# Kernel tuning notes

Hardware: AMD Instinct MI355X
Metric: run time of the kernel (lower is better)

Reference implementation:

```python
import jax, jax.numpy as jnp
import numpy as np

F_SIZE = 32
H_DIM = 540
W_DIM = 960
T_DIM = 300
HID1 = 64
FEAT = 64
HID2X2 = 256
UV_L = 10
T_L = 6
BLOCK2_IN = FEAT + (UV_L * 2 * 2 + 2) + (T_L * 2 + 1)  # 119
N_PTS = 1048576


def plane_sample(plane, uv):
    """Bilinear grid_sample, align_corners=False, padding_mode='border'.
    plane: (f, H, W); uv: (N, 2) in [0,1]; uv[:,0] samples W, uv[:,1] samples H
    (matches torch grid last-dim (x, y) convention). Returns (N, f)."""
    f, H, W = plane.shape
    g = uv * 2.0 - 1.0
    u, v = g[:, 0], g[:, 1]
    # unnormalize (align_corners=False) then border-clamp the coordinate
    ix = jnp.clip(((u + 1.0) * W - 1.0) * 0.5, 0.0, W - 1.0)
    iy = jnp.clip(((v + 1.0) * H - 1.0) * 0.5, 0.0, H - 1.0)
    x0f = jnp.floor(ix)
    y0f = jnp.floor(iy)
    wx = ix - x0f
    wy = iy - y0f
    x0 = x0f.astype(jnp.int32)
    y0 = y0f.astype(jnp.int32)
    x1 = jnp.minimum(x0 + 1, W - 1)
    y1 = jnp.minimum(y0 + 1, H - 1)
    v00 = plane[:, y0, x0]  # (f, N)
    v01 = plane[:, y0, x1]
    v10 = plane[:, y1, x0]
    v11 = plane[:, y1, x1]
    out = (v00 * (1 - wx) * (1 - wy) + v01 * wx * (1 - wy)
           + v10 * (1 - wx) * wy + v11 * wx * wy)
    return out.T  # (N, f)


def pos_enc(x, L):
    outs = [x]
    for j in range(L):
        s = (2.0 ** j) * x
        outs.append(jnp.sin(s))
        outs.append(jnp.cos(s))
    return jnp.concatenate(outs, axis=-1)


def _linear_params(key, fan_in, fan_out):
    kw, kb = jax.random.split(key)
    scale = 1.0 / np.sqrt(fan_in)
    W = jax.random.uniform(kw, (fan_in, fan_out), minval=-scale, maxval=scale, dtype=jnp.float32)
    b = jax.random.uniform(kb, (fan_out,), minval=-scale, maxval=scale, dtype=jnp.float32)
    return W, b


def setup_inputs() -> dict:
    key = jax.random.key(0)
    ks = jax.random.split(key, 10)
    xyt = jax.random.uniform(ks[0], (N_PTS, 3), dtype=jnp.float32)
    xyt = xyt.at[:, 2].multiply(300.0)  # t in [0, frames_num)
    yx_plane = jax.random.uniform(ks[1], (F_SIZE, H_DIM, W_DIM), dtype=jnp.float32)
    xt_plane = jax.random.uniform(ks[2], (F_SIZE, W_DIM, T_DIM), dtype=jnp.float32)
    yt_plane = jax.random.uniform(ks[3], (F_SIZE, H_DIM, T_DIM), dtype=jnp.float32)
    fw1, fb1 = _linear_params(ks[4], F_SIZE, HID1)
    fw2, fb2 = _linear_params(ks[5], HID1, FEAT)
    w1, b1 = _linear_params(ks[6], BLOCK2_IN, HID2X2)
    w2, b2 = _linear_params(ks[7], HID2X2, HID2X2)
    w3, b3 = _linear_params(ks[8], HID2X2, HID2X2)
    w4, b4 = _linear_params(ks[9], HID2X2, 3)
    return {"xyt": xyt, "yx_plane": yx_plane, "xt_plane": xt_plane,
            "yt_plane": yt_plane, "fw1": fw1, "fb1": fb1, "fw2": fw2,
            "fb2": fb2, "w1": w1, "b1": b1, "w2": w2, "b2": b2,
            "w3": w3, "b3": b3, "w4": w4, "b4": b4, "frames_num": 300}


def reference(xyt, yx_plane, xt_plane, yt_plane, fw1, fb1, fw2, fb2,
              w1, b1, w2, b2, w3, b3, w4, b4, frames_num):
    x = xyt[:, 0:1]
    y = xyt[:, 1:2]
    t = xyt[:, 2:3] / frames_num
    yx_f = plane_sample(yx_plane, jnp.concatenate([y, x], axis=-1))
    xt_f = plane_sample(xt_plane, jnp.concatenate([x, t], axis=-1))
    yt_f = plane_sample(yt_plane, jnp.concatenate([y, t], axis=-1))
    feat = yx_f * xt_f * yt_f  # (N, f_size)
    h = jax.nn.relu(feat @ fw1 + fb1)
    h = jax.nn.relu(h @ fw2 + fb2)
    yx_pe = pos_enc(jnp.concatenate([y, x], axis=-1), UV_L)
    t_pe = pos_enc(t, T_L)
    full = jnp.concatenate([h, yx_pe, t_pe], axis=-1)  # (N, 119)
    z = jax.nn.relu(full @ w1 + b1)
    z = jax.nn.relu(z @ w2 + b2)
    z = jax.nn.relu(z @ w3 + b3)
    colors = jax.nn.sigmoid(z @ w4 + b4)  # (N, 3)
    return colors
```

## Files before the change

kernel.cpp:

```cpp
#include <hip/hip_runtime.h>

typedef __bf16 bf16_t;
typedef __bf16 bf16x8 __attribute__((ext_vector_type(8)));
typedef _Float16 f16x4 __attribute__((ext_vector_type(4)));
typedef unsigned short u16x8 __attribute__((ext_vector_type(8)));
typedef unsigned short u16x4 __attribute__((ext_vector_type(4)));
typedef float f32x4 __attribute__((ext_vector_type(4)));

#define MT 64
#define NTHR 512
#define NBLK (1048576 / MT)

__device__ __forceinline__ int swz(int row, int colbyte) {
  return row * 512 + (colbyte ^ ((row & 31) << 4));
}
__device__ __forceinline__ void st_act(unsigned short* buf, int row, int col, float v) {
  buf[swz(row, col * 2) >> 1] = __builtin_bit_cast(unsigned short, (bf16_t)v);
}
__device__ __forceinline__ void st_act4(unsigned short* buf, int row, int col, float v0, float v1,
                                        float v2, float v3) {
  u16x4 pk;
  pk[0] = __builtin_bit_cast(unsigned short, (bf16_t)v0);
  pk[1] = __builtin_bit_cast(unsigned short, (bf16_t)v1);
  pk[2] = __builtin_bit_cast(unsigned short, (bf16_t)v2);
  pk[3] = __builtin_bit_cast(unsigned short, (bf16_t)v3);
  *reinterpret_cast<uint2*>(reinterpret_cast<char*>(buf) + swz(row, col * 2)) =
      __builtin_bit_cast(uint2, pk);
}
__device__ __forceinline__ bf16x8 ld_frag(const unsigned short* buf, int row, int kbyte) {
  const uint4 u =
      *reinterpret_cast<const uint4*>(reinterpret_cast<const char*>(buf) + swz(row, kbyte));
  return __builtin_bit_cast(bf16x8, u);
}

__global__ void KPlanes_tr3(const float* __restrict__ yx, const float* __restrict__ xt,
                            const float* __restrict__ yt, uint4* __restrict__ d0,
                            uint4* __restrict__ d1, uint4* __restrict__ d2) {
  const int HW0 = 518400, HW1 = 288000, HW2 = 162000;
  const int NB0 = 2025, NB1 = 1125;
  const int b = blockIdx.x;
  const float* src;
  uint4* dst;
  int HW, s;
  if (b < NB0) {
    src = yx; dst = d0; HW = HW0; s = b * 256 + threadIdx.x;
  } else if (b < NB0 + NB1) {
    src = xt; dst = d1; HW = HW1; s = (b - NB0) * 256 + threadIdx.x;
  } else {
    src = yt; dst = d2; HW = HW2; s = (b - NB0 - NB1) * 256 + threadIdx.x;
  }
  if (s >= HW) return;
#pragma unroll
  for (int g = 0; g < 4; ++g) {
    u16x8 v;
#pragma unroll
    for (int j = 0; j < 8; ++j) {
      const float w = src[(size_t)(g * 8 + j) * HW + s];
      v[j] = __builtin_bit_cast(unsigned short, (_Float16)w);
    }
    dst[(size_t)s * 4 + g] = __builtin_bit_cast(uint4, v);
  }
}

__global__ void KPlanes_packall(const float* __restrict__ fw1, const float* __restrict__ fw2,
                                const float* __restrict__ w1, const float* __restrict__ w2,
                                const float* __restrict__ w3, const float* __restrict__ w4,
                                uint4* __restrict__ dst) {
  const int F = blockIdx.x * 4 + (threadIdx.x >> 6);
  const int lane = threadIdx.x & 63;
  if (F >= 340) return;
  const float* W;
  int N, K, KS, fbase;
  if (F < 4)        { W = fw1; N = 64;  K = 32;  KS = 1; fbase = 0; }
  else if (F < 12)  { W = fw2; N = 64;  K = 64;  KS = 2; fbase = 4; }
  else if (F < 76)  { W = w1;  N = 256; K = 119; KS = 4; fbase = 12; }
  else if (F < 204) { W = w2;  N = 256; K = 256; KS = 8; fbase = 76; }
  else if (F < 332) { W = w3;  N = 256; K = 256; KS = 8; fbase = 204; }
  else              { W = w4;  N = 3;   K = 256; KS = 8; fbase = 332; }
  const int f = F - fbase;
  const int g = f / KS, ks = f - g * KS;
  const int col = g * 16 + (lane & 15);
  u16x8 v;
#pragma unroll
  for (int j = 0; j < 8; ++j) {
    const int k = ks * 32 + (lane >> 4) * 8 + j;
    const float w = (k < K && col < N) ? W[(size_t)k * N + col] : 0.0f;
    v[j] = __builtin_bit_cast(unsigned short, (bf16_t)w);
  }
  dst[(size_t)F * 64 + lane] = __builtin_bit_cast(uint4, v);
}

struct Smp4 {
  uint2 c00, c01, c10, c11;
  float w00, w01, w10, w11;
};
__device__ __forceinline__ Smp4 sample_ld4(const uint2* __restrict__ plt, int Hd, int Wd, float u,
                                           float v, int q) {
  Smp4 s;
  float ix = fminf(fmaxf(u * (float)Wd - 0.5f, 0.f), (float)Wd - 1.f);
  float iy = fminf(fmaxf(v * (float)Hd - 0.5f, 0.f), (float)Hd - 1.f);
  float x0f = floorf(ix), y0f = floorf(iy);
  float wx = ix - x0f, wy = iy - y0f;
  int x0 = (int)x0f, y0 = (int)y0f;
  int x1 = min(x0 + 1, Wd - 1), y1 = min(y0 + 1, Hd - 1);
  s.w00 = (1.f - wx) * (1.f - wy);
  s.w01 = wx * (1.f - wy);
  s.w10 = (1.f - wx) * wy;
  s.w11 = wx * wy;
  const size_t r0 = (size_t)y0 * Wd, r1 = (size_t)y1 * Wd;
  s.c00 = plt[(r0 + x0) * 8 + q];
  s.c01 = plt[(r0 + x1) * 8 + q];
  s.c10 = plt[(r1 + x0) * 8 + q];
  s.c11 = plt[(r1 + x1) * 8 + q];
  return s;
}
__device__ __forceinline__ void smp_combine4(const Smp4& s, float* o) {
  const f16x4 a = __builtin_bit_cast(f16x4, s.c00);
  const f16x4 b = __builtin_bit_cast(f16x4, s.c01);
  const f16x4 c = __builtin_bit_cast(f16x4, s.c10);
  const f16x4 d = __builtin_bit_cast(f16x4, s.c11);
#pragma unroll
  for (int i = 0; i < 4; ++i)
    o[i] = (float)a[i] * s.w00 + (float)b[i] * s.w01 + (float)c[i] * s.w10 + (float)d[i] * s.w11;
}

template <int KS, int NT, int MTPW, bool RELU>
__device__ __forceinline__ void layer_pp(const unsigned short* in, unsigned short* outb,
                                         const uint4* __restrict__ Wf,
                                         const float* __restrict__ bg, int gbase, int moff,
                                         int lane) {
  const int l15 = lane & 15, lhi = lane >> 4;
  f32x4 acc[MTPW][NT];
#pragma unroll
  for (int m = 0; m < MTPW; ++m)
#pragma unroll
    for (int t = 0; t < NT; ++t) acc[m][t] = f32x4{0.f, 0.f, 0.f, 0.f};
#pragma unroll
  for (int ks = 0; ks < KS; ++ks) {
    bf16x8 wa[NT];
#pragma unroll
    for (int t = 0; t < NT; ++t)
      wa[t] = __builtin_bit_cast(bf16x8, Wf[(size_t)((gbase + t) * KS + ks) * 64 + lane]);
#pragma unroll
    for (int m = 0; m < MTPW; ++m) {
      const bf16x8 b = ld_frag(in, (moff + m) * 16 + l15, ks * 64 + lhi * 16);
#pragma unroll
      for (int t = 0; t < NT; ++t)
        acc[m][t] = __builtin_amdgcn_mfma_f32_16x16x32_bf16(wa[t], b, acc[m][t], 0, 0, 0);
    }
  }
#pragma unroll
  for (int t = 0; t < NT; ++t) {
    const int ncol = (gbase + t) * 16 + lhi * 4;
    const float4 b4 = *reinterpret_cast<const float4*>(&bg[ncol]);
#pragma unroll
    for (int m = 0; m < MTPW; ++m) {
      const int row = (moff + m) * 16 + l15;
      float v0 = acc[m][t][0] + b4.x, v1 = acc[m][t][1] + b4.y;
      float v2 = acc[m][t][2] + b4.z, v3 = acc[m][t][3] + b4.w;
      if (RELU) {
        v0 = fmaxf(v0, 0.f); v1 = fmaxf(v1, 0.f);
        v2 = fmaxf(v2, 0.f); v3 = fmaxf(v3, 0.f);
      }
      st_act4(outb, row, ncol, v0, v1, v2, v3);
    }
  }
}

__global__ __launch_bounds__(NTHR, 4) void KPlanes_fused6(
    const float* __restrict__ xyt, const uint2* __restrict__ yx_h, const uint2* __restrict__ xt_h,
    const uint2* __restrict__ yt_h, const uint4* __restrict__ wf1, const float* __restrict__ fb1,
    const uint4* __restrict__ wf2, const float* __restrict__ fb2, const uint4* __restrict__ wf3,
    const float* __restrict__ b1, const uint4* __restrict__ wf4, const float* __restrict__ b2,
    const uint4* __restrict__ wf5, const float* __restrict__ b3, const uint4* __restrict__ wf6,
    const float* __restrict__ b4, const int* __restrict__ fnum_p, float* __restrict__ out) {
  __shared__ unsigned short actA[MT * 256];
  __shared__ unsigned short actB[MT * 256];
  const int tid = threadIdx.x;
  const int lane = tid & 63;
  const int wid = tid >> 6;
  const float rfn = 1.0f / (float)(*fnum_p);

  {
    const int p = tid >> 3;
    const int q = tid & 7;
    const int pg = blockIdx.x * MT + p;
    const float x = xyt[pg * 3 + 0];
    const float y = xyt[pg * 3 + 1];
    const float t = xyt[pg * 3 + 2] * rfn;
    Smp4 sYX = sample_ld4(yx_h, 540, 960, y, x, q);
    Smp4 sXT = sample_ld4(xt_h, 960, 300, x, t, q);
    Smp4 sYT = sample_ld4(yt_h, 540, 300, y, t, q);
    if (q == 4) {
      st_act(actA, p, 64, y);
      float sj, cj;
      sincosf(y, &sj, &cj);
#pragma unroll
      for (int j = 0; j < 10; ++j) {
        st_act(actA, p, 66 + j * 4, sj);
        st_act(actA, p, 68 + j * 4, cj);
        const float ns = 2.f * sj * cj;
        cj = fmaf(-2.f * sj, sj, 1.f);
        sj = ns;
      }
    } else if (q == 5) {
      st_act(actA, p, 65, x);
      float sj, cj;
      sincosf(x, &sj, &cj);
#pragma unroll
      for (int j = 0; j < 10; ++j) {
        st_act(actA, p, 67 + j * 4, sj);
        st_act(actA, p, 69 + j * 4, cj);
        const float ns = 2.f * sj * cj;
        cj = fmaf(-2.f * sj, sj, 1.f);
        sj = ns;
      }
    } else if (q == 6) {
      st_act(actA, p, 106, t);
      float sj, cj;
      sincosf(t, &sj, &cj);
#pragma unroll
      for (int j = 0; j < 6; ++j) {
        st_act(actA, p, 107 + 2 * j, sj);
        st_act(actA, p, 108 + 2 * j, cj);
        const float ns = 2.f * sj * cj;
        cj = fmaf(-2.f * sj, sj, 1.f);
        sj = ns;
      }
    } else if (q == 7) {
      st_act(actA, p, 119, 0.f);
      st_act4(actA, p, 120, 0.f, 0.f, 0.f, 0.f);
      st_act4(actA, p, 124, 0.f, 0.f, 0.f, 0.f);
    }
    float a4[4], b4_[4], c4[4];
    smp_combine4(sYX, a4);
    smp_combine4(sXT, b4_);
    smp_combine4(sYT, c4);
    st_act4(actA, p, q * 4, a4[0] * b4_[0] * c4[0], a4[1] * b4_[1] * c4[1],
            a4[2] * b4_[2] * c4[2], a4[3] * b4_[3] * c4[3]);
  }
  __syncthreads();
  layer_pp<1, 1, 2, true>(actA, actB, wf1, fb1, wid & 3, (wid >> 2) * 2, lane);
  __syncthreads();
  layer_pp<2, 1, 2, true>(actB, actA, wf2, fb2, wid & 3, (wid >> 2) * 2, lane);
  __syncthreads();
  layer_pp<4, 2, 4, true>(actA, actB, wf3, b1, wid * 2, 0, lane);
  __syncthreads();
  layer_pp<8, 2, 4, true>(actB, actA, wf4, b2, wid * 2, 0, lane);
  __syncthreads();
  layer_pp<8, 2, 4, true>(actA, actB, wf5, b3, wid * 2, 0, lane);
  __syncthreads();
  if (wid < 4) {
    const int l15 = lane & 15, lhi = lane >> 4;
    f32x4 acc = {0.f, 0.f, 0.f, 0.f};
#pragma unroll
    for (int ks = 0; ks < 8; ++ks) {
      const bf16x8 wa = __builtin_bit_cast(bf16x8, wf6[ks * 64 + lane]);
      acc = __builtin_amdgcn_mfma_f32_16x16x32_bf16(
          wa, ld_frag(actB, wid * 16 + l15, ks * 64 + lhi * 16), acc, 0, 0, 0);
    }
    if (lhi == 0) {
      const size_t pg = (size_t)blockIdx.x * MT + wid * 16 + l15;
#pragma unroll
      for (int i = 0; i < 3; ++i) {
        const float v = acc[i] + b4[i];
        out[pg * 3 + i] = 1.f / (1.f + expf(-v));
      }
    }
  }
}

__device__ __forceinline__ void sample8_f(const float* __restrict__ pl, int Hd, int Wd, float u,
                                          float v, int cgrp, float* o) {
  float ix = fminf(fmaxf(u * (float)Wd - 0.5f, 0.f), (float)Wd - 1.f);
  float iy = fminf(fmaxf(v * (float)Hd - 0.5f, 0.f), (float)Hd - 1.f);
  float x0f = floorf(ix), y0f = floorf(iy);
  float wx = ix - x0f, wy = iy - y0f;
  int x0 = (int)x0f, y0 = (int)y0f;
  int x1 = min(x0 + 1, Wd - 1), y1 = min(y0 + 1, Hd - 1);
  float w00 = (1.f - wx) * (1.f - wy), w01 = wx * (1.f - wy);
  float w10 = (1.f - wx) * wy, w11 = wx * wy;
  const size_t HW = (size_t)Hd * Wd;
#pragma unroll
  for (int i = 0; i < 8; ++i) {
    const float* bc = pl + (size_t)(cgrp + i) * HW;
    float a = bc[(size_t)y0 * Wd + x0], b = bc[(size_t)y0 * Wd + x1];
    float c = bc[(size_t)y1 * Wd + x0], d = bc[(size_t)y1 * Wd + x1];
    o[i] = a * w00 + b * w01 + c * w10 + d * w11;
  }
}

template <int KSTEPS, int NCPW, bool RELU>
__device__ __forceinline__ void mfma_layer_fb(const unsigned short* inb, unsigned short* outb,
                                              const float* __restrict__ Wg,
                                              const float* __restrict__ bg, int N, int Kmax,
                                              int wid, int lane) {
  const int l15 = lane & 15;
  const int lhi = lane >> 4;
#pragma unroll
  for (int t = 0; t < NCPW; ++t) {
    const int nc = wid * NCPW + t;
    const int col = nc * 16 + l15;
    const float bias = bg[col];
    bf16x8 bfrag[KSTEPS];
#pragma unroll
    for (int ks = 0; ks < KSTEPS; ++ks) {
#pragma unroll
      for (int j = 0; j < 8; ++j) {
        const int k = ks * 32 + lhi * 8 + j;
        float wv = (k < Kmax) ? Wg[(size_t)k * N + col] : 0.0f;
        bfrag[ks][j] = (bf16_t)wv;
      }
    }
#pragma unroll
    for (int m = 0; m < 4; ++m) {
      f32x4 acc = {0.f, 0.f, 0.f, 0.f};
#pragma unroll
      for (int ks = 0; ks < KSTEPS; ++ks) {
        bf16x8 a = ld_frag(inb, m * 16 + l15, ks * 64 + lhi * 16);
        acc = __builtin_amdgcn_mfma_f32_16x16x32_bf16(a, bfrag[ks], acc, 0, 0, 0);
      }
      const int r0 = m * 16 + lhi * 4;
#pragma unroll
      for (int i = 0; i < 4; ++i) {
        float v = acc[i] + bias;
        if (RELU) v = fmaxf(v, 0.f);
        st_act(outb, r0 + i, col, v);
      }
    }
  }
}

__global__ __launch_bounds__(256) void KPlanes_fused_fb(
    const float* __restrict__ xyt, const float* __restrict__ yx, const float* __restrict__ xt,
    const float* __restrict__ yt, const float* __restrict__ fw1, const float* __restrict__ fb1,
    const float* __restrict__ fw2, const float* __restrict__ fb2, const float* __restrict__ w1,
    const float* __restrict__ b1, const float* __restrict__ w2, const float* __restrict__ b2,
    const float* __restrict__ w3, const float* __restrict__ b3, const float* __restrict__ w4,
    const float* __restrict__ b4, const int* __restrict__ fnum_p, float* __restrict__ out) {
  __shared__ unsigned short actA[64 * 256];
  __shared__ unsigned short actB[64 * 256];
  const int tid = threadIdx.x;
  const int lane = tid & 63;
  const int wid = tid >> 6;
  const float fnum = (float)(*fnum_p);
  {
    const int p = tid >> 2;
    const int cgrp = (tid & 3) * 8;
    const int pg = blockIdx.x * 64 + p;
    float x = xyt[pg * 3 + 0];
    float y = xyt[pg * 3 + 1];
    float t = xyt[pg * 3 + 2] / fnum;
    float syx[8], sxt[8], syt[8];
    sample8_f(yx, 540, 960, y, x, cgrp, syx);
    sample8_f(xt, 960, 300, x, t, cgrp, sxt);
    sample8_f(yt, 540, 300, y, t, cgrp, syt);
#pragma unroll
    for (int i = 0; i < 8; ++i) st_act(actA, p, cgrp + i, syx[i] * sxt[i] * syt[i]);
  }
  __syncthreads();
  mfma_layer_fb<1, 1, true>(actA, actB, fw1, fb1, 64, 32, wid, lane);
  __syncthreads();
  mfma_layer_fb<2, 1, true>(actB, actA, fw2, fb2, 64, 64, wid, lane);
  if (tid < 64) {
    const int pg = blockIdx.x * 64 + tid;
    float px = xyt[pg * 3 + 0];
    float py = xyt[pg * 3 + 1];
    float pt = xyt[pg * 3 + 2] / fnum;
    st_act(actA, tid, 64, py);
    st_act(actA, tid, 65, px);
    float sc = 1.f;
#pragma unroll
    for (int j = 0; j < 10; ++j) {
      st_act(actA, tid, 66 + j * 4 + 0, sinf(sc * py));
      st_act(actA, tid, 66 + j * 4 + 1, sinf(sc * px));
      st_act(actA, tid, 66 + j * 4 + 2, cosf(sc * py));
      st_act(actA, tid, 66 + j * 4 + 3, cosf(sc * px));
      sc *= 2.f;
    }
    st_act(actA, tid, 106, pt);
    sc = 1.f;
#pragma unroll
    for (int j = 0; j < 6; ++j) {
      st_act(actA, tid, 107 + j * 2, sinf(sc * pt));
      st_act(actA, tid, 108 + j * 2, cosf(sc * pt));
      sc *= 2.f;
    }
#pragma unroll
    for (int c = 119; c < 128; ++c) st_act(actA, tid, c, 0.f);
  }
  __syncthreads();
  mfma_layer_fb<4, 4, true>(actA, actB, w1, b1, 256, 119, wid, lane);
  __syncthreads();
  mfma_layer_fb<8, 4, true>(actB, actA, w2, b2, 256, 256, wid, lane);
  __syncthreads();
  mfma_layer_fb<8, 4, true>(actA, actB, w3, b3, 256, 256, wid, lane);
  __syncthreads();
  {
    const int p = tid >> 2, c = tid & 3;
    if (c < 3) {
      float acc = 0.f;
#pragma unroll
      for (int k0 = 0; k0 < 256; k0 += 8) {
        int b = swz(p, k0 * 2);
        uint4 u = *reinterpret_cast<const uint4*>(reinterpret_cast<const char*>(actB) + b);
        bf16x8 z = __builtin_bit_cast(bf16x8, u);
#pragma unroll
        for (int j = 0; j < 8; ++j) acc += (float)z[j] * w4[(k0 + j) * 3 + c];
      }
      acc += b4[c];
      out[(size_t)(blockIdx.x * 64 + p) * 3 + c] = 1.f / (1.f + expf(-acc));
    }
  }
}

extern "C" void kernel_launch(void* const* d_in, const int* in_sizes, int n_in, void* d_out,
                              int out_size, void* d_ws, size_t ws_size, hipStream_t stream) {
  const float* xyt = (const float*)d_in[0];
  const float* yx = (const float*)d_in[1];
  const float* xt = (const float*)d_in[2];
  const float* yt = (const float*)d_in[3];
  const float* fw1 = (const float*)d_in[4];
  const float* fb1 = (const float*)d_in[5];
  const float* fw2 = (const float*)d_in[6];
  const float* fb2 = (const float*)d_in[7];
  const float* w1 = (const float*)d_in[8];
  const float* b1 = (const float*)d_in[9];
  const float* w2 = (const float*)d_in[10];
  const float* b2 = (const float*)d_in[11];
  const float* w3 = (const float*)d_in[12];
  const float* b3 = (const float*)d_in[13];
  const float* w4 = (const float*)d_in[14];
  const float* b4 = (const float*)d_in[15];
  const int* fnum = (const int*)d_in[16];
  float* out = (float*)d_out;

  const int hw_yx = 540 * 960, hw_xt = 960 * 300, hw_yt = 540 * 300;
  const size_t plane_bytes = ((size_t)hw_yx + hw_xt + hw_yt) * 64;
  const size_t wfrag_bytes = (size_t)340 * 64 * sizeof(uint4);
  const size_t need = plane_bytes + wfrag_bytes;

  char* ws = (char*)d_ws;
  uint2* yx_h = (uint2*)ws;
  uint2* xt_h = (uint2*)(ws + (size_t)hw_yx * 64);
  uint2* yt_h = (uint2*)(ws + (size_t)(hw_yx + hw_xt) * 64);
  uint4* wbase = (uint4*)(ws + plane_bytes);
  uint4* wf1 = wbase + 0 * 64;
  uint4* wf2 = wbase + 4 * 64;
  uint4* wf3 = wbase + 12 * 64;
  uint4* wf4 = wbase + 76 * 64;
  uint4* wf5 = wbase + 204 * 64;
  uint4* wf6 = wbase + 332 * 64;

  if (ws_size >= need) {
    const int nb_tr = 2025 + 1125 + 633;
    KPlanes_tr3<<<nb_tr, 256, 0, stream>>>(yx, xt, yt, (uint4*)yx_h, (uint4*)xt_h, (uint4*)yt_h);
    KPlanes_packall<<<85, 256, 0, stream>>>(fw1, fw2, w1, w2, w3, w4, wbase);
    KPlanes_fused6<<<NBLK, NTHR, 0, stream>>>(xyt, yx_h, xt_h, yt_h, wf1, fb1, wf2, fb2, wf3, b1,
                                              wf4, b2, wf5, b3, wf6, b4, fnum, out);
  } else {
    KPlanes_fused_fb<<<1048576 / 64, 256, 0, stream>>>(xyt, yx, xt, yt, fw1, fb1, fw2, fb2, w1,
                                                       b1, w2, b2, w3, b3, w4, b4, fnum, out);
  }
}
```

Before: 476.9 us.

## Store MLP activations in LDS as pre-packed MFMA fragments instead of swizzled rows

```diff
diff --git a/kernel.cpp b/kernel.cpp
--- a/kernel.cpp
+++ b/kernel.cpp
@@ -11,26 +11,21 @@
 #define NTHR 512
 #define NBLK (1048576 / MT)
 
-__device__ __forceinline__ int swz(int row, int colbyte) {
-  return row * 512 + (colbyte ^ ((row & 31) << 4));
-}
-__device__ __forceinline__ void st_act(unsigned short* buf, int row, int col, float v) {
-  buf[swz(row, col * 2) >> 1] = __builtin_bit_cast(unsigned short, (bf16_t)v);
-}
-__device__ __forceinline__ void st_act4(unsigned short* buf, int row, int col, float v0, float v1,
-                                        float v2, float v3) {
+__device__ __forceinline__ int fragoff(int NK, int pg, int n, int p15) {
+  return ((pg * NK + (n >> 5)) << 10) + (((n >> 3) & 3) << 8) + (p15 << 4) + ((n & 7) << 1);
+}
+__device__ __forceinline__ void st_frag1(char* buf, int NK, int pg, int n, int p15, float v) {
+  *reinterpret_cast<unsigned short*>(buf + fragoff(NK, pg, n, p15)) =
+      __builtin_bit_cast(unsigned short, (bf16_t)v);
+}
+__device__ __forceinline__ void st_frag4(char* buf, int NK, int pg, int n, int p15, float v0,
+                                         float v1, float v2, float v3) {
   u16x4 pk;
   pk[0] = __builtin_bit_cast(unsigned short, (bf16_t)v0);
   pk[1] = __builtin_bit_cast(unsigned short, (bf16_t)v1);
   pk[2] = __builtin_bit_cast(unsigned short, (bf16_t)v2);
   pk[3] = __builtin_bit_cast(unsigned short, (bf16_t)v3);
-  *reinterpret_cast<uint2*>(reinterpret_cast<char*>(buf) + swz(row, col * 2)) =
-      __builtin_bit_cast(uint2, pk);
-}
-__device__ __forceinline__ bf16x8 ld_frag(const unsigned short* buf, int row, int kbyte) {
-  const uint4 u =
-      *reinterpret_cast<const uint4*>(reinterpret_cast<const char*>(buf) + swz(row, kbyte));
-  return __builtin_bit_cast(bf16x8, u);
+  *reinterpret_cast<uint2*>(buf + fragoff(NK, pg, n, p15)) = __builtin_bit_cast(uint2, pk);
 }
 
 __global__ void KPlanes_tr3(const float* __restrict__ yx, const float* __restrict__ xt,
@@ -124,12 +119,12 @@
     o[i] = (float)a[i] * s.w00 + (float)b[i] * s.w01 + (float)c[i] * s.w10 + (float)d[i] * s.w11;
 }
 
-template <int KS, int NT, int MTPW, bool RELU>
-__device__ __forceinline__ void layer_pp(const unsigned short* in, unsigned short* outb,
-                                         const uint4* __restrict__ Wf,
+template <int KS, int NKOUT, int NT, int MTPW, bool RELU>
+__device__ __forceinline__ void layer_fp(const char* in, char* outb, const uint4* __restrict__ Wf,
                                          const float* __restrict__ bg, int gbase, int moff,
                                          int lane) {
   const int l15 = lane & 15, lhi = lane >> 4;
+  const char* rb = in + lane * 16 + moff * (KS << 10);
   f32x4 acc[MTPW][NT];
 #pragma unroll
   for (int m = 0; m < MTPW; ++m)
@@ -143,7 +138,8 @@
       wa[t] = __builtin_bit_cast(bf16x8, Wf[(size_t)((gbase + t) * KS + ks) * 64 + lane]);
 #pragma unroll
     for (int m = 0; m < MTPW; ++m) {
-      const bf16x8 b = ld_frag(in, (moff + m) * 16 + l15, ks * 64 + lhi * 16);
+      const uint4 u = *reinterpret_cast<const uint4*>(rb + ((m * KS + ks) << 10));
+      const bf16x8 b = __builtin_bit_cast(bf16x8, u);
 #pragma unroll
       for (int t = 0; t < NT; ++t)
         acc[m][t] = __builtin_amdgcn_mfma_f32_16x16x32_bf16(wa[t], b, acc[m][t], 0, 0, 0);
@@ -152,30 +148,29 @@
 #pragma unroll
   for (int t = 0; t < NT; ++t) {
     const int ncol = (gbase + t) * 16 + lhi * 4;
-    const float4 b4 = *reinterpret_cast<const float4*>(&bg[ncol]);
+    const float4 bb = *reinterpret_cast<const float4*>(&bg[ncol]);
 #pragma unroll
     for (int m = 0; m < MTPW; ++m) {
-      const int row = (moff + m) * 16 + l15;
-      float v0 = acc[m][t][0] + b4.x, v1 = acc[m][t][1] + b4.y;
-      float v2 = acc[m][t][2] + b4.z, v3 = acc[m][t][3] + b4.w;
+      float v0 = acc[m][t][0] + bb.x, v1 = acc[m][t][1] + bb.y;
+      float v2 = acc[m][t][2] + bb.z, v3 = acc[m][t][3] + bb.w;
       if (RELU) {
         v0 = fmaxf(v0, 0.f); v1 = fmaxf(v1, 0.f);
         v2 = fmaxf(v2, 0.f); v3 = fmaxf(v3, 0.f);
       }
-      st_act4(outb, row, ncol, v0, v1, v2, v3);
-    }
-  }
-}
-
-__global__ __launch_bounds__(NTHR, 4) void KPlanes_fused6(
+      st_frag4(outb, NKOUT, moff + m, ncol, l15, v0, v1, v2, v3);
+    }
+  }
+}
+
+__global__ __launch_bounds__(NTHR, 4) void KPlanes_fused7(
     const float* __restrict__ xyt, const uint2* __restrict__ yx_h, const uint2* __restrict__ xt_h,
     const uint2* __restrict__ yt_h, const uint4* __restrict__ wf1, const float* __restrict__ fb1,
     const uint4* __restrict__ wf2, const float* __restrict__ fb2, const uint4* __restrict__ wf3,
     const float* __restrict__ b1, const uint4* __restrict__ wf4, const float* __restrict__ b2,
     const uint4* __restrict__ wf5, const float* __restrict__ b3, const uint4* __restrict__ wf6,
     const float* __restrict__ b4, const int* __restrict__ fnum_p, float* __restrict__ out) {
-  __shared__ unsigned short actA[MT * 256];
-  __shared__ unsigned short actB[MT * 256];
+  __shared__ char actS[32768];
+  __shared__ char actB[32768];
   const int tid = threadIdx.x;
   const int lane = tid & 63;
   const int wid = tid >> 6;
@@ -184,92 +179,104 @@
   {
     const int p = tid >> 3;
     const int q = tid & 7;
-    const int pg = blockIdx.x * MT + p;
-    const float x = xyt[pg * 3 + 0];
-    const float y = xyt[pg * 3 + 1];
-    const float t = xyt[pg * 3 + 2] * rfn;
+    const int pg = p >> 4, p15 = p & 15;
+    const int pgl = blockIdx.x * MT + p;
+    const float x = xyt[pgl * 3 + 0];
+    const float y = xyt[pgl * 3 + 1];
+    const float t = xyt[pgl * 3 + 2] * rfn;
     Smp4 sYX = sample_ld4(yx_h, 540, 960, y, x, q);
     Smp4 sXT = sample_ld4(xt_h, 960, 300, x, t, q);
     Smp4 sYT = sample_ld4(yt_h, 540, 300, y, t, q);
     if (q == 4) {
-      st_act(actA, p, 64, y);
+      st_frag1(actS, 4, pg, 64, p15, y);
       float sj, cj;
       sincosf(y, &sj, &cj);
 #pragma unroll
       for (int j = 0; j < 10; ++j) {
-        st_act(actA, p, 66 + j * 4, sj);
-        st_act(actA, p, 68 + j * 4, cj);
+        st_frag1(actS, 4, pg, 66 + j * 4, p15, sj);
+        st_frag1(actS, 4, pg, 68 + j * 4, p15, cj);
         const float ns = 2.f * sj * cj;
         cj = fmaf(-2.f * sj, sj, 1.f);
         sj = ns;
       }
     } else if (q == 5) {
-      st_act(actA, p, 65, x);
+      st_frag1(actS, 4, pg, 65, p15, x);
       float sj, cj;
       sincosf(x, &sj, &cj);
 #pragma unroll
       for (int j = 0; j < 10; ++j) {
-        st_act(actA, p, 67 + j * 4, sj);
-        st_act(actA, p, 69 + j * 4, cj);
+        st_frag1(actS, 4, pg, 67 + j * 4, p15, sj);
+        st_frag1(actS, 4, pg, 69 + j * 4, p15, cj);
         const float ns = 2.f * sj * cj;
         cj = fmaf(-2.f * sj, sj, 1.f);
         sj = ns;
       }
     } else if (q == 6) {
-      st_act(actA, p, 106, t);
+      st_frag1(actS, 4, pg, 106, p15, t);
       float sj, cj;
       sincosf(t, &sj, &cj);
 #pragma unroll
       for (int j = 0; j < 6; ++j) {
-        st_act(actA, p, 107 + 2 * j, sj);
-        st_act(actA, p, 108 + 2 * j, cj);
+        st_frag1(actS, 4, pg, 107 + 2 * j, p15, sj);
+        st_frag1(actS, 4, pg, 108 + 2 * j, p15, cj);
         const float ns = 2.f * sj * cj;
         cj = fmaf(-2.f * sj, sj, 1.f);
         sj = ns;
       }
     } else if (q == 7) {
-      st_act(actA, p, 119, 0.f);
-      st_act4(actA, p, 120, 0.f, 0.f, 0.f, 0.f);
-      st_act4(actA, p, 124, 0.f, 0.f, 0.f, 0.f);
+      st_frag1(actS, 4, pg, 119, p15, 0.f);
+      *reinterpret_cast<uint4*>(actS + fragoff(4, pg, 120, p15)) = uint4{0u, 0u, 0u, 0u};
     }
     float a4[4], b4_[4], c4[4];
     smp_combine4(sYX, a4);
     smp_combine4(sXT, b4_);
     smp_combine4(sYT, c4);
-    st_act4(actA, p, q * 4, a4[0] * b4_[0] * c4[0], a4[1] * b4_[1] * c4[1],
-            a4[2] * b4_[2] * c4[2], a4[3] * b4_[3] * c4[3]);
-  }
-  __syncthreads();
-  layer_pp<1, 1, 2, true>(actA, actB, wf1, fb1, wid & 3, (wid >> 2) * 2, lane);
-  __syncthreads();
-  layer_pp<2, 1, 2, true>(actB, actA, wf2, fb2, wid & 3, (wid >> 2) * 2, lane);
-  __syncthreads();
-  layer_pp<4, 2, 4, true>(actA, actB, wf3, b1, wid * 2, 0, lane);
-  __syncthreads();
-  layer_pp<8, 2, 4, true>(actB, actA, wf4, b2, wid * 2, 0, lane);
-  __syncthreads();
-  layer_pp<8, 2, 4, true>(actA, actB, wf5, b3, wid * 2, 0, lane);
+    st_frag4(actS + 16384, 1, pg, q * 4, p15, a4[0] * b4_[0] * c4[0], a4[1] * b4_[1] * c4[1],
+             a4[2] * b4_[2] * c4[2], a4[3] * b4_[3] * c4[3]);
+  }
+  __syncthreads();
+  layer_fp<1, 2, 1, 2, true>(actS + 16384, actB, wf1, fb1, wid & 3, (wid >> 2) * 2, lane);
+  __syncthreads();
+  layer_fp<2, 4, 1, 2, true>(actB, actS, wf2, fb2, wid & 3, (wid >> 2) * 2, lane);
+  __syncthreads();
+  layer_fp<4, 8, 2, 4, true>(actS, actB, wf3, b1, wid * 2, 0, lane);
+  __syncthreads();
+  layer_fp<8, 8, 2, 4, true>(actB, actS, wf4, b2, wid * 2, 0, lane);
+  __syncthreads();
+  layer_fp<8, 8, 2, 4, true>(actS, actB, wf5, b3, wid * 2, 0, lane);
   __syncthreads();
   if (wid < 4) {
     const int l15 = lane & 15, lhi = lane >> 4;
+    const char* rb = actB + lane * 16 + wid * 8192;
     f32x4 acc = {0.f, 0.f, 0.f, 0.f};
 #pragma unroll
     for (int ks = 0; ks < 8; ++ks) {
       const bf16x8 wa = __builtin_bit_cast(bf16x8, wf6[ks * 64 + lane]);
-      acc = __builtin_amdgcn_mfma_f32_16x16x32_bf16(
-          wa, ld_frag(actB, wid * 16 + l15, ks * 64 + lhi * 16), acc, 0, 0, 0);
+      const bf16x8 b = __builtin_bit_cast(bf16x8, *reinterpret_cast<const uint4*>(rb + (ks << 10)));
+      acc = __builtin_amdgcn_mfma_f32_16x16x32_bf16(wa, b, acc, 0, 0, 0);
     }
     if (lhi == 0) {
-      const size_t pg = (size_t)blockIdx.x * MT + wid * 16 + l15;
+      const size_t pgl = (size_t)blockIdx.x * MT + wid * 16 + l15;
 #pragma unroll
       for (int i = 0; i < 3; ++i) {
         const float v = acc[i] + b4[i];
-        out[pg * 3 + i] = 1.f / (1.f + expf(-v));
-      }
-    }
-  }
-}
-
+        out[pgl * 3 + i] = 1.f / (1.f + expf(-v));
+      }
+    }
+  }
+}
+
+__device__ __forceinline__ int swz(int row, int colbyte) {
+  return row * 512 + (colbyte ^ ((row & 31) << 4));
+}
+__device__ __forceinline__ void st_act(unsigned short* buf, int row, int col, float v) {
+  buf[swz(row, col * 2) >> 1] = __builtin_bit_cast(unsigned short, (bf16_t)v);
+}
+__device__ __forceinline__ bf16x8 ld_frag(const unsigned short* buf, int row, int kbyte) {
+  const uint4 u =
+      *reinterpret_cast<const uint4*>(reinterpret_cast<const char*>(buf) + swz(row, kbyte));
+  return __builtin_bit_cast(bf16x8, u);
+}
 __device__ __forceinline__ void sample8_f(const float* __restrict__ pl, int Hd, int Wd, float u,
                                           float v, int cgrp, float* o) {
   float ix = fminf(fmaxf(u * (float)Wd - 0.5f, 0.f), (float)Wd - 1.f);
@@ -456,7 +463,7 @@
     const int nb_tr = 2025 + 1125 + 633;
     KPlanes_tr3<<<nb_tr, 256, 0, stream>>>(yx, xt, yt, (uint4*)yx_h, (uint4*)xt_h, (uint4*)yt_h);
     KPlanes_packall<<<85, 256, 0, stream>>>(fw1, fw2, w1, w2, w3, w4, wbase);
-    KPlanes_fused6<<<NBLK, NTHR, 0, stream>>>(xyt, yx_h, xt_h, yt_h, wf1, fb1, wf2, fb2, wf3, b1,
+    KPlanes_fused7<<<NBLK, NTHR, 0, stream>>>(xyt, yx_h, xt_h, yt_h, wf1, fb1, wf2, fb2, wf3, b1,
                                               wf4, b2, wf5, b3, wf6, b4, fnum, out);
   } else {
     KPlanes_fused_fb<<<1048576 / 64, 256, 0, stream>>>(xyt, yx, xt, yt, fw1, fb1, fw2, fb2, w1,
```

Result: no change. 477.2 us (+0.1%).
